# Optimization experiments

Measured on AMD Instinct MI355X. Metric: run time of the kernel, lower is better.

Reference implementation:

```python
import jax, jax.numpy as jnp
import numpy as np

DIM = 1024
NUM_HEADS = 16
HEAD_DIM = DIM // NUM_HEADS
SCALE = HEAD_DIM ** -0.5


def setup_inputs() -> dict:
    key = jax.random.key(0)
    k1, k2, k3, k4 = jax.random.split(key, 4)
    x = jax.random.normal(k1, (4, 2048, DIM), dtype=jnp.float32)
    # torch nn.Linear(dim, 3*dim, bias=False): weight shape [3*dim, dim]
    w_qkv = jax.random.normal(k2, (3 * DIM, DIM), dtype=jnp.float32) * (DIM ** -0.5)
    # torch nn.Linear(dim, dim): weight [dim, dim], bias [dim]
    w_proj = jax.random.normal(k3, (DIM, DIM), dtype=jnp.float32) * (DIM ** -0.5)
    b_proj = jax.random.normal(k4, (DIM,), dtype=jnp.float32) * 0.01
    return {"x": x, "w_qkv": w_qkv, "w_proj": w_proj, "b_proj": b_proj}


def reference(x, w_qkv, w_proj, b_proj):
    B, N, C = x.shape
    # qkv: [B, N, 3*C] -> [3, B, H, N, Dh]
    qkv = (x @ w_qkv.T).reshape(B, N, 3, NUM_HEADS, HEAD_DIM)
    qkv = jnp.transpose(qkv, (2, 0, 3, 1, 4))
    q, k, v = qkv[0], qkv[1], qkv[2]
    # full score matrix, as in the original module
    attn = jnp.einsum("bhqd,bhkd->bhqk", q, k) * SCALE
    attn = jax.nn.softmax(attn, axis=-1)
    out = jnp.einsum("bhqk,bhkd->bhqd", attn, v)  # [B,H,N,Dh]
    out = jnp.transpose(out, (0, 2, 1, 3)).reshape(B, N, C)
    return out @ w_proj.T + b_proj
```

## Files before the change

### kernel.cpp

```cpp
#include <hip/hip_runtime.h>
#include <stdint.h>

#define DIM 1024
#define SEQ 2048
#define BATCH 4
#define ROWS (BATCH*SEQ)
#define SCALE 0.125f

typedef __attribute__((ext_vector_type(8))) short bf16x8;
typedef __attribute__((ext_vector_type(4))) float f32x4;

__device__ __forceinline__ unsigned short f2bf(float f) {
  union { float f; unsigned int u; } v; v.f = f;
  unsigned int u = v.u;
  return (unsigned short)((u + 0x7FFFu + ((u >> 16) & 1u)) >> 16);
}

__device__ __forceinline__ void gload_lds16(const void* g, void* l) {
  __builtin_amdgcn_global_load_lds(
      (const __attribute__((address_space(1))) unsigned int*)g,
      (__attribute__((address_space(3))) unsigned int*)l,
      16, 0, 0);
}

__global__ void cast_f32_bf16(const float* __restrict__ src,
                              unsigned short* __restrict__ dst, int n) {
  int i = (blockIdx.x * blockDim.x + threadIdx.x) * 4;
  if (i < n) {
    float4 f = *(const float4*)(src + i);
    ushort4 o;
    o.x = f2bf(f.x); o.y = f2bf(f.y); o.z = f2bf(f.z); o.w = f2bf(f.w);
    *(ushort4*)(dst + i) = o;
  }
}

__global__ __launch_bounds__(256) void gemm_qkv(
    const unsigned short* __restrict__ A,
    const unsigned short* __restrict__ W,
    unsigned short* __restrict__ qb,
    unsigned short* __restrict__ kb,
    unsigned short* __restrict__ vtb) {
  const int M = ROWS, N = 3 * DIM, K = DIM;
  __shared__ unsigned short Al[128 * 32];
  __shared__ unsigned short Wl[128 * 32];
  const int tid  = threadIdx.x;
  const int wave = tid >> 6, lane = tid & 63;
  const int quad = lane >> 4, l16 = lane & 15;
  const int m0 = blockIdx.y * 128, n0 = blockIdx.x * 128;
  const int wr = (wave >> 1) * 64, wc = (wave & 1) * 64;

  f32x4 acc[4][4];
#pragma unroll
  for (int i = 0; i < 4; i++)
#pragma unroll
    for (int j = 0; j < 4; j++) acc[i][j] = (f32x4)0.f;

  const int arow = wave * 16 + (lane >> 2);
  const int acol = (lane & 3) * 8;
  const unsigned short* Ag = A + (size_t)(m0 + arow) * K + acol;
  const unsigned short* Wg = W + (size_t)(n0 + arow) * K + acol;

  for (int kt = 0; kt < K; kt += 32) {
    __syncthreads();
#pragma unroll
    for (int i = 0; i < 2; i++) {
      gload_lds16((const void*)(Ag + (size_t)(i * 64) * K + kt), (void*)&Al[i * 2048 + wave * 512]);
      gload_lds16((const void*)(Wg + (size_t)(i * 64) * K + kt), (void*)&Wl[i * 2048 + wave * 512]);
    }
    __syncthreads();

    bf16x8 af[4], wf[4];
#pragma unroll
    for (int i = 0; i < 4; i++) {
      af[i] = *(const bf16x8*)&Al[(wr + i * 16 + l16) * 32 + quad * 8];
      wf[i] = *(const bf16x8*)&Wl[(wc + i * 16 + l16) * 32 + quad * 8];
    }
#pragma unroll
    for (int i = 0; i < 4; i++)
#pragma unroll
      for (int j = 0; j < 4; j++)
        acc[i][j] = __builtin_amdgcn_mfma_f32_16x16x32_bf16(af[i], wf[j], acc[i][j], 0, 0, 0);
  }

#pragma unroll
  for (int i = 0; i < 4; i++) {
    const int row = m0 + wr + i * 16 + quad * 4;
    const int b = row >> 11;
    const int n = row & 2047;
#pragma unroll
    for (int j = 0; j < 4; j++) {
      const int col = n0 + wc + j * 16 + l16;
      const int which = col >> 10;
      const int h = (col >> 6) & 15;
      const int d = col & 63;
      const int bh = b * 16 + h;
      if (which == 2) {
        ushort4 o4;
        o4.x = f2bf(acc[i][j][0]); o4.y = f2bf(acc[i][j][1]);
        o4.z = f2bf(acc[i][j][2]); o4.w = f2bf(acc[i][j][3]);
        *(ushort4*)&vtb[((size_t)bh * 64 + d) * SEQ + n] = o4;
      } else {
        unsigned short* dst = (which == 0 ? qb : kb) + ((size_t)bh * SEQ + n) * 64 + d;
#pragma unroll
        for (int r = 0; r < 4; r++) dst[r * 64] = f2bf(acc[i][j][r]);
      }
    }
  }
}

__global__ __launch_bounds__(256, 4) void attn_kernel(
    const unsigned short* __restrict__ qb,
    const unsigned short* __restrict__ kb,
    const unsigned short* __restrict__ vtb,
    unsigned short* __restrict__ out) {
  __shared__ unsigned short Kl[64 * 64];
  __shared__ unsigned short Vl[64 * 64];
  __shared__ unsigned short Pb[4][32 * 64];

  const int tid  = threadIdx.x;
  const int wave = tid >> 6, lane = tid & 63;
  const int quad = lane >> 4, l16 = lane & 15;
  const int qtile = blockIdx.x;
  const int bh    = blockIdx.y;
  const size_t qkbase = (size_t)bh * SEQ * 64;
  const size_t vtbase = (size_t)bh * 64 * SEQ;
  const int q0 = qtile * 128 + wave * 32;

  bf16x8 qf[2][2];
#pragma unroll
  for (int mi = 0; mi < 2; mi++)
#pragma unroll
    for (int kk = 0; kk < 2; kk++)
      qf[mi][kk] = *(const bf16x8*)&qb[qkbase + (size_t)(q0 + mi * 16 + l16) * 64 + kk * 32 + quad * 8];

  f32x4 o[2][4];
#pragma unroll
  for (int mi = 0; mi < 2; mi++)
#pragma unroll
    for (int nt = 0; nt < 4; nt++) o[mi][nt] = (f32x4)0.f;
  float lp[2][4];
#pragma unroll
  for (int mi = 0; mi < 2; mi++)
#pragma unroll
    for (int r = 0; r < 4; r++) lp[mi][r] = 0.f;

  const unsigned short* Kg = kb + qkbase;
  const unsigned short* Vg = vtb + vtbase;
  const int srow = tid >> 3;
  const int schk = tid & 7;

  for (int kt = 0; kt < SEQ; kt += 64) {
    __syncthreads();
#pragma unroll
    for (int p = 0; p < 2; p++) {
      const int r = p * 32 + srow;
      const int sw = schk ^ (r & 7);
      gload_lds16((const void*)(Kg + (size_t)(kt + r) * 64 + sw * 8),
                  (void*)&Kl[p * 2048 + wave * 512]);
      gload_lds16((const void*)(Vg + (size_t)r * SEQ + kt + sw * 8),
                  (void*)&Vl[p * 2048 + wave * 512]);
    }
    __syncthreads();

#pragma unroll
    for (int nh = 0; nh < 4; nh++) {
      const int R = nh * 16 + l16;
      const int sb = R & 7;
      bf16x8 kf0 = *(const bf16x8*)&Kl[R * 64 + ((quad ^ sb) << 3)];
      bf16x8 kf1 = *(const bf16x8*)&Kl[R * 64 + (((4 + quad) ^ sb) << 3)];
#pragma unroll
      for (int mi = 0; mi < 2; mi++) {
        f32x4 s = (f32x4)0.f;
        s = __builtin_amdgcn_mfma_f32_16x16x32_bf16(qf[mi][0], kf0, s, 0, 0, 0);
        s = __builtin_amdgcn_mfma_f32_16x16x32_bf16(qf[mi][1], kf1, s, 0, 0, 0);
#pragma unroll
        for (int r = 0; r < 4; r++) {
          const float e = __expf(s[r] * SCALE);
          lp[mi][r] += e;
          const int ql = mi * 16 + quad * 4 + r;
          Pb[wave][ql * 64 + (((nh * 2 + (l16 >> 3)) ^ (ql & 7)) << 3) + (l16 & 7)] = f2bf(e);
        }
      }
    }

#pragma unroll
    for (int kk = 0; kk < 2; kk++) {
      bf16x8 pf[2];
#pragma unroll
      for (int mi = 0; mi < 2; mi++) {
        const int R = mi * 16 + l16;
        pf[mi] = *(const bf16x8*)&Pb[wave][R * 64 + (((kk * 4 + quad) ^ (R & 7)) << 3)];
      }
#pragma unroll
      for (int nt = 0; nt < 4; nt++) {
        const int R = nt * 16 + l16;
        bf16x8 vf = *(const bf16x8*)&Vl[R * 64 + (((kk * 4 + quad) ^ (R & 7)) << 3)];
        o[0][nt] = __builtin_amdgcn_mfma_f32_16x16x32_bf16(pf[0], vf, o[0][nt], 0, 0, 0);
        o[1][nt] = __builtin_amdgcn_mfma_f32_16x16x32_bf16(pf[1], vf, o[1][nt], 0, 0, 0);
      }
    }
  }

#pragma unroll
  for (int mi = 0; mi < 2; mi++)
#pragma unroll
    for (int r = 0; r < 4; r++) {
      float v = lp[mi][r];
#pragma unroll
      for (int m = 1; m < 16; m <<= 1) v += __shfl_xor(v, m, 64);
      lp[mi][r] = 1.f / v;
    }

  const int h = bh & 15, b = bh >> 4;
#pragma unroll
  for (int mi = 0; mi < 2; mi++)
#pragma unroll
    for (int nt = 0; nt < 4; nt++)
#pragma unroll
      for (int r = 0; r < 4; r++)
        out[((size_t)(b * SEQ + q0 + mi * 16 + quad * 4 + r)) * DIM + h * 64 + nt * 16 + l16] =
            f2bf(o[mi][nt][r] * lp[mi][r]);
}

__global__ __launch_bounds__(256) void gemm_proj(
    const unsigned short* __restrict__ A,
    const unsigned short* __restrict__ W,
    float* __restrict__ out,
    const float* __restrict__ bias) {
  const int N = DIM, K = DIM;
  __shared__ unsigned short Al[128 * 32];
  __shared__ unsigned short Wl[128 * 32];
  const int tid  = threadIdx.x;
  const int wave = tid >> 6, lane = tid & 63;
  const int quad = lane >> 4, l16 = lane & 15;
  const int m0 = blockIdx.y * 128, n0 = blockIdx.x * 128;
  const int wr = (wave >> 1) * 64, wc = (wave & 1) * 64;

  f32x4 acc[4][4];
#pragma unroll
  for (int i = 0; i < 4; i++)
#pragma unroll
    for (int j = 0; j < 4; j++) acc[i][j] = (f32x4)0.f;

  const int arow = wave * 16 + (lane >> 2);
  const int acol = (lane & 3) * 8;
  const unsigned short* Ag = A + (size_t)(m0 + arow) * K + acol;
  const unsigned short* Wg = W + (size_t)(n0 + arow) * K + acol;

  for (int kt = 0; kt < K; kt += 32) {
    __syncthreads();
#pragma unroll
    for (int i = 0; i < 2; i++) {
      gload_lds16((const void*)(Ag + (size_t)(i * 64) * K + kt), (void*)&Al[i * 2048 + wave * 512]);
      gload_lds16((const void*)(Wg + (size_t)(i * 64) * K + kt), (void*)&Wl[i * 2048 + wave * 512]);
    }
    __syncthreads();

    bf16x8 af[4], wf[4];
#pragma unroll
    for (int i = 0; i < 4; i++) {
      af[i] = *(const bf16x8*)&Al[(wr + i * 16 + l16) * 32 + quad * 8];
      wf[i] = *(const bf16x8*)&Wl[(wc + i * 16 + l16) * 32 + quad * 8];
    }
#pragma unroll
    for (int i = 0; i < 4; i++)
#pragma unroll
      for (int j = 0; j < 4; j++)
        acc[i][j] = __builtin_amdgcn_mfma_f32_16x16x32_bf16(af[i], wf[j], acc[i][j], 0, 0, 0);
  }

#pragma unroll
  for (int i = 0; i < 4; i++) {
    const int row = m0 + wr + i * 16 + quad * 4;
#pragma unroll
    for (int j = 0; j < 4; j++) {
      const int col = n0 + wc + j * 16 + l16;
      const float bv = bias[col];
#pragma unroll
      for (int r = 0; r < 4; r++)
        out[(size_t)(row + r) * N + col] = acc[i][j][r] + bv;
    }
  }
}

extern "C" void kernel_launch(void* const* d_in, const int* in_sizes, int n_in,
                              void* d_out, int out_size, void* d_ws, size_t ws_size,
                              hipStream_t stream) {
  const float* x      = (const float*)d_in[0];
  const float* w_qkv  = (const float*)d_in[1];
  const float* w_proj = (const float*)d_in[2];
  const float* b_proj = (const float*)d_in[3];
  float* outp = (float*)d_out;

  char* ws = (char*)d_ws;
  unsigned short* xb     = (unsigned short*)(ws);
  unsigned short* wqkvb  = (unsigned short*)(ws + (16u << 20));
  unsigned short* wprojb = (unsigned short*)(ws + (22u << 20));
  unsigned short* qb     = (unsigned short*)(ws + (24u << 20));
  unsigned short* kb     = (unsigned short*)(ws + (40u << 20));
  unsigned short* vtb    = (unsigned short*)(ws + (56u << 20));
  unsigned short* aout   = (unsigned short*)(ws + (72u << 20));

  cast_f32_bf16<<<ROWS * DIM / 1024, 256, 0, stream>>>(x, xb, ROWS * DIM);
  cast_f32_bf16<<<3 * DIM * DIM / 1024, 256, 0, stream>>>(w_qkv, wqkvb, 3 * DIM * DIM);
  cast_f32_bf16<<<DIM * DIM / 1024, 256, 0, stream>>>(w_proj, wprojb, DIM * DIM);

  gemm_qkv<<<dim3(24, 64), 256, 0, stream>>>(xb, wqkvb, qb, kb, vtb);
  attn_kernel<<<dim3(16, 64), 256, 0, stream>>>(qb, kb, vtb, aout);
  gemm_proj<<<dim3(8, 64), 256, 0, stream>>>(aout, wprojb, outp, b_proj);
}
```

Before: 294.7 us.

## Double attention query tile, fold scale into Q, and sum softmax via MFMA

Each wave now handles 64 query rows instead of 32, so every K/V tile loaded into LDS serves twice as many queries and the grid is halved. The softmax scale and log2(e) are folded into Q when the QKV GEMM writes it, so attention can use a raw exp2. The score MFMA operands are swapped so P is written to LDS as packed, truncated bf16 vectors. Row sums now come from an MFMA against a ones vector instead of scalar adds and shuffles. The cost is more registers and a larger P buffer (launch bounds drop to 2), and truncating P to bf16 and summing those rounded values slightly changes numerics.

After: 285.9 us. 3.0% less time.

```diff
diff --git a/kernel.cpp b/kernel.cpp
--- a/kernel.cpp
+++ b/kernel.cpp
@@ -5,15 +5,27 @@
 #define SEQ 2048
 #define BATCH 4
 #define ROWS (BATCH*SEQ)
-#define SCALE 0.125f
+#define QSCALE 0.1803368801111f
 
 typedef __attribute__((ext_vector_type(8))) short bf16x8;
 typedef __attribute__((ext_vector_type(4))) float f32x4;
+
+#if __has_builtin(__builtin_amdgcn_exp2f)
+#define EXP2F(x) __builtin_amdgcn_exp2f(x)
+#else
+#define EXP2F(x) __expf((x) * 0.69314718056f)
+#endif
 
 __device__ __forceinline__ unsigned short f2bf(float f) {
   union { float f; unsigned int u; } v; v.f = f;
   unsigned int u = v.u;
   return (unsigned short)((u + 0x7FFFu + ((u >> 16) & 1u)) >> 16);
+}
+
+__device__ __forceinline__ unsigned int pack_bf16_trunc(float lo, float hi) {
+  union { float f; unsigned int u; } a, b;
+  a.f = lo; b.f = hi;
+  return __builtin_amdgcn_perm(b.u, a.u, 0x07060302u);
 }
 
 __device__ __forceinline__ void gload_lds16(const void* g, void* l) {
@@ -40,7 +52,7 @@
     unsigned short* __restrict__ qb,
     unsigned short* __restrict__ kb,
     unsigned short* __restrict__ vtb) {
-  const int M = ROWS, N = 3 * DIM, K = DIM;
+  const int K = DIM;
   __shared__ unsigned short Al[128 * 32];
   __shared__ unsigned short Wl[128 * 32];
   const int tid  = threadIdx.x;
@@ -99,8 +111,12 @@
         o4.x = f2bf(acc[i][j][0]); o4.y = f2bf(acc[i][j][1]);
         o4.z = f2bf(acc[i][j][2]); o4.w = f2bf(acc[i][j][3]);
         *(ushort4*)&vtb[((size_t)bh * 64 + d) * SEQ + n] = o4;
+      } else if (which == 0) {
+        unsigned short* dst = qb + ((size_t)bh * SEQ + n) * 64 + d;
+#pragma unroll
+        for (int r = 0; r < 4; r++) dst[r * 64] = f2bf(acc[i][j][r] * QSCALE);
       } else {
-        unsigned short* dst = (which == 0 ? qb : kb) + ((size_t)bh * SEQ + n) * 64 + d;
+        unsigned short* dst = kb + ((size_t)bh * SEQ + n) * 64 + d;
 #pragma unroll
         for (int r = 0; r < 4; r++) dst[r * 64] = f2bf(acc[i][j][r]);
       }
@@ -108,14 +124,14 @@
   }
 }
 
-__global__ __launch_bounds__(256, 4) void attn_kernel(
+__global__ __launch_bounds__(256, 2) void attn_kernel(
     const unsigned short* __restrict__ qb,
     const unsigned short* __restrict__ kb,
     const unsigned short* __restrict__ vtb,
     unsigned short* __restrict__ out) {
   __shared__ unsigned short Kl[64 * 64];
   __shared__ unsigned short Vl[64 * 64];
-  __shared__ unsigned short Pb[4][32 * 64];
+  __shared__ unsigned short Pb[4][64 * 64];
 
   const int tid  = threadIdx.x;
   const int wave = tid >> 6, lane = tid & 63;
@@ -123,29 +139,30 @@
   const int qtile = blockIdx.x;
   const int bh    = blockIdx.y;
   const size_t qkbase = (size_t)bh * SEQ * 64;
-  const size_t vtbase = (size_t)bh * 64 * SEQ;
-  const int q0 = qtile * 128 + wave * 32;
-
-  bf16x8 qf[2][2];
-#pragma unroll
-  for (int mi = 0; mi < 2; mi++)
+  const int q0 = qtile * 256 + wave * 64;
+
+  bf16x8 qf[4][2];
+#pragma unroll
+  for (int mi = 0; mi < 4; mi++)
 #pragma unroll
     for (int kk = 0; kk < 2; kk++)
       qf[mi][kk] = *(const bf16x8*)&qb[qkbase + (size_t)(q0 + mi * 16 + l16) * 64 + kk * 32 + quad * 8];
 
-  f32x4 o[2][4];
-#pragma unroll
-  for (int mi = 0; mi < 2; mi++)
+  f32x4 o[4][4];
+#pragma unroll
+  for (int mi = 0; mi < 4; mi++)
 #pragma unroll
     for (int nt = 0; nt < 4; nt++) o[mi][nt] = (f32x4)0.f;
-  float lp[2][4];
-#pragma unroll
-  for (int mi = 0; mi < 2; mi++)
-#pragma unroll
-    for (int r = 0; r < 4; r++) lp[mi][r] = 0.f;
+  f32x4 lacc[4];
+#pragma unroll
+  for (int mi = 0; mi < 4; mi++) lacc[mi] = (f32x4)0.f;
+
+  bf16x8 ones;
+#pragma unroll
+  for (int j = 0; j < 8; j++) ones[j] = (short)0x3F80;
 
   const unsigned short* Kg = kb + qkbase;
-  const unsigned short* Vg = vtb + vtbase;
+  const unsigned short* Vg = vtb + (size_t)bh * 64 * SEQ;
   const int srow = tid >> 3;
   const int schk = tid & 7;
 
@@ -169,57 +186,54 @@
       bf16x8 kf0 = *(const bf16x8*)&Kl[R * 64 + ((quad ^ sb) << 3)];
       bf16x8 kf1 = *(const bf16x8*)&Kl[R * 64 + (((4 + quad) ^ sb) << 3)];
 #pragma unroll
-      for (int mi = 0; mi < 2; mi++) {
+      for (int mi = 0; mi < 4; mi++) {
         f32x4 s = (f32x4)0.f;
-        s = __builtin_amdgcn_mfma_f32_16x16x32_bf16(qf[mi][0], kf0, s, 0, 0, 0);
-        s = __builtin_amdgcn_mfma_f32_16x16x32_bf16(qf[mi][1], kf1, s, 0, 0, 0);
-#pragma unroll
-        for (int r = 0; r < 4; r++) {
-          const float e = __expf(s[r] * SCALE);
-          lp[mi][r] += e;
-          const int ql = mi * 16 + quad * 4 + r;
-          Pb[wave][ql * 64 + (((nh * 2 + (l16 >> 3)) ^ (ql & 7)) << 3) + (l16 & 7)] = f2bf(e);
-        }
+        s = __builtin_amdgcn_mfma_f32_16x16x32_bf16(kf0, qf[mi][0], s, 0, 0, 0);
+        s = __builtin_amdgcn_mfma_f32_16x16x32_bf16(kf1, qf[mi][1], s, 0, 0, 0);
+        const float e0 = EXP2F(s[0]), e1 = EXP2F(s[1]);
+        const float e2 = EXP2F(s[2]), e3 = EXP2F(s[3]);
+        uint2 pk;
+        pk.x = pack_bf16_trunc(e0, e1);
+        pk.y = pack_bf16_trunc(e2, e3);
+        const int q = mi * 16 + l16;
+        const int chunk = (nh * 2 + (quad >> 1)) ^ (l16 & 7);
+        *(uint2*)&Pb[wave][q * 64 + (chunk << 3) + ((quad & 1) << 2)] = pk;
       }
     }
 
 #pragma unroll
     for (int kk = 0; kk < 2; kk++) {
-      bf16x8 pf[2];
-#pragma unroll
-      for (int mi = 0; mi < 2; mi++) {
-        const int R = mi * 16 + l16;
-        pf[mi] = *(const bf16x8*)&Pb[wave][R * 64 + (((kk * 4 + quad) ^ (R & 7)) << 3)];
-      }
+      bf16x8 vf[4];
 #pragma unroll
       for (int nt = 0; nt < 4; nt++) {
         const int R = nt * 16 + l16;
-        bf16x8 vf = *(const bf16x8*)&Vl[R * 64 + (((kk * 4 + quad) ^ (R & 7)) << 3)];
-        o[0][nt] = __builtin_amdgcn_mfma_f32_16x16x32_bf16(pf[0], vf, o[0][nt], 0, 0, 0);
-        o[1][nt] = __builtin_amdgcn_mfma_f32_16x16x32_bf16(pf[1], vf, o[1][nt], 0, 0, 0);
+        vf[nt] = *(const bf16x8*)&Vl[R * 64 + (((kk * 4 + quad) ^ (R & 7)) << 3)];
       }
-    }
-  }
-
-#pragma unroll
-  for (int mi = 0; mi < 2; mi++)
-#pragma unroll
-    for (int r = 0; r < 4; r++) {
-      float v = lp[mi][r];
-#pragma unroll
-      for (int m = 1; m < 16; m <<= 1) v += __shfl_xor(v, m, 64);
-      lp[mi][r] = 1.f / v;
-    }
+#pragma unroll
+      for (int mi = 0; mi < 4; mi++) {
+        const int R = mi * 16 + l16;
+        bf16x8 pf = *(const bf16x8*)&Pb[wave][R * 64 + (((kk * 4 + quad) ^ (l16 & 7)) << 3)];
+        lacc[mi] = __builtin_amdgcn_mfma_f32_16x16x32_bf16(pf, ones, lacc[mi], 0, 0, 0);
+#pragma unroll
+        for (int nt = 0; nt < 4; nt++)
+          o[mi][nt] = __builtin_amdgcn_mfma_f32_16x16x32_bf16(pf, vf[nt], o[mi][nt], 0, 0, 0);
+      }
+    }
+  }
 
   const int h = bh & 15, b = bh >> 4;
 #pragma unroll
-  for (int mi = 0; mi < 2; mi++)
+  for (int mi = 0; mi < 4; mi++) {
+    float inv[4];
+#pragma unroll
+    for (int r = 0; r < 4; r++) inv[r] = 1.f / lacc[mi][r];
 #pragma unroll
     for (int nt = 0; nt < 4; nt++)
 #pragma unroll
       for (int r = 0; r < 4; r++)
         out[((size_t)(b * SEQ + q0 + mi * 16 + quad * 4 + r)) * DIM + h * 64 + nt * 16 + l16] =
-            f2bf(o[mi][nt][r] * lp[mi][r]);
+            f2bf(o[mi][nt][r] * inv[r]);
+  }
 }
 
 __global__ __launch_bounds__(256) void gemm_proj(
@@ -306,6 +320,6 @@
   cast_f32_bf16<<<DIM * DIM / 1024, 256, 0, stream>>>(w_proj, wprojb, DIM * DIM);
 
   gemm_qkv<<<dim3(24, 64), 256, 0, stream>>>(xb, wqkvb, qb, kb, vtb);
-  attn_kernel<<<dim3(16, 64), 256, 0, stream>>>(qb, kb, vtb, aout);
+  attn_kernel<<<dim3(8, 64), 256, 0, stream>>>(qb, kb, vtb, aout);
   gemm_proj<<<dim3(8, 64), 256, 0, stream>>>(aout, wprojb, outp, b_proj);
 }
```
